# Performance work log

Hardware: AMD Instinct MI355X
Metric: run time of the kernel (lower is better)

The kernel has to match this reference:

```python
import jax, jax.numpy as jnp
import numpy as np
from jax.scipy.special import gammaln

EPS = 1e-8
N_SAMPLES = 2 ** 17
ATTACK_FULL_SIZE = 2048
CPD = 16
N_RES = 16
EXPR = 2
N_OSC = 2
N_GAUSS = 8
N_EVENTS = 4
FRAMES = 128
DEF_FRAMES = 128
N_LEVELS = 11  # log2(ATTACK_FULL_SIZE)


def unit_norm(x, axis=-1):
    return x / (jnp.linalg.norm(x, axis=axis, keepdims=True) + EPS)


def fft_convolve(a, b):
    # zero-pad to 2n to avoid circular wraparound, multiply spectra, crop to n
    n = a.shape[-1]
    fa = jnp.fft.rfft(a, n=2 * n, axis=-1)
    fb = jnp.fft.rfft(b, n=2 * n, axis=-1)
    return jnp.fft.irfft(fa * fb, n=2 * n, axis=-1)[..., :n]


def upsample_with_holes(x, size):
    # zero-insertion upsampling: place frames at stride `factor`
    factor = size // x.shape[-1]
    out = jnp.zeros(x.shape[:-1] + (size,), x.dtype)
    return out.at[..., ::factor].set(x)


def interpolate_last_axis(x, size):
    # linear interpolation, align_corners=False semantics (torch F.interpolate)
    n = x.shape[-1]
    scale = n / size
    src = jnp.clip((jnp.arange(size) + 0.5) * scale - 0.5, 0.0, n - 1.0)
    lo = jnp.floor(src).astype(jnp.int32)
    hi = jnp.minimum(lo + 1, n - 1)
    w = (src - lo).astype(x.dtype)
    return x[..., lo] * (1.0 - w) + x[..., hi] * w


def ensure_last_axis_length(x, size):
    n = x.shape[-1]
    if n == size:
        return x
    if n > size:
        return x[..., :size]
    return jnp.pad(x, [(0, 0)] * (x.ndim - 1) + [(0, size - n)])


def sparse_softmax(x):
    # hard one-hot forward, softmax straight-through backward
    sm = jax.nn.softmax(x, axis=-1)
    hard = jax.nn.one_hot(jnp.argmax(x, axis=-1), x.shape[-1], dtype=x.dtype)
    return hard + sm - jax.lax.stop_gradient(sm)


def hierarchical_dirac(p):
    # p: (..., L, 2) binary choices per level -> one-hot dirac of length 2**L
    sel = sparse_softmax(p)
    sig = sel[..., 0, :]
    for i in range(1, p.shape[-2]):
        sig = (sig[..., :, None] * sel[..., i, :][..., None, :]).reshape(*sig.shape[:-1], -1)
    return sig


def gamma_pdf(mean, std, n_elements):
    # gamma pdf on support (eps, 1], parameterized by mean/std
    t = jnp.linspace(EPS, 1.0, n_elements)
    k = (mean / (std + EPS)) ** 2
    rate = mean / (std ** 2 + EPS)
    k = k[..., None]
    rate = rate[..., None]
    logp = k * jnp.log(rate + EPS) + (k - 1.0) * jnp.log(t) - rate * t - gammaln(k)
    return jnp.exp(logp)


def damped_harmonic_oscillator(time, mass, damping, tension, x0):
    # underdamped closed-form solution, v0 = 0
    omega0_sq = tension / mass
    gamma = damping / (2.0 * mass)
    omega = jnp.sqrt(omega0_sq - gamma ** 2)
    A = x0
    B = gamma * x0 / omega
    return jnp.exp(-gamma * time) * (A * jnp.cos(omega * time) + B * jnp.sin(omega * time))


def dho_block(damping, mass, tension, disp, amps, tmod=None, scaling=None):
    time = jnp.linspace(0.0, 10.0, N_SAMPLES).reshape(1, 1, 1, N_SAMPLES)
    t = tension[..., None]  # (N_OSC, N_RES, EXPR, 1)
    if tmod is not None:
        t = t + tmod[0] * scaling  # broadcast -> (N_OSC, N_RES, EXPR, N_SAMPLES)
    x = damped_harmonic_oscillator(
        time,
        jax.nn.sigmoid(mass[..., None]) * 2.0,
        jax.nn.sigmoid(damping[..., None]) * 30.0,
        10.0 ** t,
        disp[..., None],
    )
    x = (x * amps).sum(axis=0)  # sum over oscillators
    return x.reshape(1, 1, N_RES, EXPR, N_SAMPLES)


def attack_envelopes(means, stds, amps, pos, overall_amp):
    m, s, a = jnp.abs(means), jnp.abs(stds), jnp.abs(amps)
    p = hierarchical_dirac(pos)  # (1,1,CPD,NG,2048)
    x = gamma_pdf(m, s, ATTACK_FULL_SIZE) * a[..., None]
    x = fft_convolve(x, p)
    x = x.sum(axis=2)  # (1,1,NG,2048)
    x = unit_norm(x)
    x = x * overall_amp[..., None]  # broadcast -> (1,1,CPD,NG,2048)
    x = x.sum(axis=-2)  # (1,1,CPD,2048)
    return x.reshape(CPD, ATTACK_FULL_SIZE)


def _forward(control_signal, deformations, ae_means, ae_stds, ae_amps, ae_pos,
             ae_overall_amp, dho_damping, dho_mass, dho_tension, dho_disp, dho_amp,
             influences, stack_mix, router, layer_mix, gains, attack_noise):
    b, ne, cpd, frames = control_signal.shape
    # --- DampedHarmonicOscillatorStack ---
    o1 = dho_block(dho_damping[0], dho_mass[0], dho_tension[0], dho_disp[0], dho_amp[0])
    o2 = dho_block(dho_damping[1], dho_mass[1], dho_tension[1], dho_disp[1], dho_amp[1], o1, influences[0])
    o3 = dho_block(dho_damping[2], dho_mass[2], dho_tension[2], dho_disp[2], dho_amp[2], o2, influences[1])
    res = (jnp.stack([o1, o2, o3], axis=-1) * jax.nn.softmax(stack_mix, axis=-1)).sum(axis=-1)
    res = unit_norm(res)
    # --- AttackEnvelopes ---
    ae = attack_envelopes(ae_means, ae_stds, ae_amps, ae_pos, ae_overall_amp)
    # --- execute_layer ---
    routed = jnp.einsum('becf,cr->berf', control_signal, router)
    before = routed
    res = unit_norm(res)  # execute_layer normalizes again
    routed = upsample_with_holes(routed.reshape(b, ne, N_RES, 1, frames), N_SAMPLES)
    # ae.shape[-1] == window_size, so materialize_attack_envelopes just multiplies noise
    impulse = ensure_last_axis_length(ae * attack_noise, N_SAMPLES).reshape(1, 1, cpd, 1, N_SAMPLES)
    routed = fft_convolve(impulse, routed)  # (1,ne,N_RES,1,S)
    cs = routed.reshape(1, ne, cpd, N_SAMPLES).sum(axis=1, keepdims=True)
    conv = fft_convolve(routed, res)  # (1,ne,N_RES,EXPR,S)
    base = jnp.zeros_like(deformations).at[:, :, 0:1, :].set(1.0)
    d = jax.nn.softmax(base + deformations, axis=-2)
    d = interpolate_last_axis(d.reshape(b, 1, 1, EXPR, -1), N_SAMPLES)
    x = (d * conv).sum(axis=-2)  # (1,ne,N_RES,S)
    mixes = jax.nn.softmax(layer_mix.reshape(1, 1, N_RES, 1, 1, 2), axis=-1)
    stacked = jnp.stack([routed, x.reshape(routed.shape)], axis=-1)
    x = (mixes * stacked).sum(axis=-1)
    x = x.reshape(1, 1, N_RES, -1)
    summed = jnp.tanh(x * jnp.abs(gains.reshape(1, 1, N_RES, 1)))
    summed = summed.sum(axis=-2, keepdims=True)
    return summed, before, cs


def setup_inputs() -> dict:
    key = jax.random.key(0)
    ks = jax.random.split(key, 20)
    u = lambda k, shape, lo, hi: jax.random.uniform(k, shape, jnp.float32, lo, hi)
    inp = {}
    inp['control_signal'] = jax.random.uniform(ks[0], (1, N_EVENTS, CPD, FRAMES), jnp.float32)
    inp['deformations'] = jax.random.normal(ks[1], (1, 1, EXPR, DEF_FRAMES), jnp.float32)
    inp['ae_means'] = u(ks[2], (1, 1, CPD, N_GAUSS), -6.0, 6.0)
    inp['ae_stds'] = u(ks[3], (1, 1, CPD, N_GAUSS), 0.5, 6.0)
    inp['ae_amps'] = u(ks[4], (1, 1, CPD, N_GAUSS), -6.0, 6.0)
    inp['ae_pos'] = u(ks[5], (1, 1, CPD, N_GAUSS, N_LEVELS, 2), -1.0, 1.0)
    inp['ae_overall_amp'] = u(ks[6], (1, 1, CPD, 1), -1.0, 1.0)
    inp['dho_damping'] = u(ks[7], (3, N_OSC, N_RES, EXPR), 0.5, 1.5)
    inp['dho_mass'] = u(ks[8], (3, N_OSC, N_RES, EXPR), -2.0, 2.0)
    inp['dho_tension'] = u(ks[9], (3, N_OSC, N_RES, EXPR), 4.0, 9.0)
    inp['dho_disp'] = u(ks[10], (3, N_OSC, N_RES, EXPR), -1.0, 2.0)
    inp['dho_amp'] = u(ks[11], (3, N_OSC, N_RES, EXPR, 1), -1.0, 1.0)
    inp['influences'] = u(ks[12], (2, N_OSC, N_RES, EXPR, 1), -0.01, 0.01)
    inp['stack_mix'] = u(ks[13], (1, 1, N_RES, EXPR, 1, 3), -1.0, 1.0)
    router = u(ks[14], (CPD, N_RES), -1.0, 1.0)
    mask = (jax.random.uniform(ks[15], (CPD, N_RES)) < 0.1).astype(jnp.float32)
    inp['router'] = router * mask
    inp['layer_mix'] = u(ks[16], (N_RES, 2), -1.0, 1.0)
    inp['gains'] = u(ks[17], (N_RES, 1), 0.01, 1.1)
    inp['attack_noise'] = u(ks[18], (CPD, ATTACK_FULL_SIZE), -1.0, 1.0)
    return inp


def reference(control_signal, deformations, ae_means, ae_stds, ae_amps, ae_pos,
              ae_overall_amp, dho_damping, dho_mass, dho_tension, dho_disp, dho_amp,
              influences, stack_mix, router, layer_mix, gains, attack_noise):
    return _forward(control_signal, deformations, ae_means, ae_stds, ae_amps, ae_pos,
                    ae_overall_amp, dho_damping, dho_mass, dho_tension, dho_disp, dho_amp,
                    influences, stack_mix, router, layer_mix, gains, attack_noise)
```

## Files before the change

### kernel.cpp

```cpp
#include <hip/hip_runtime.h>
#include <math.h>

#define NS 131072
#define EPSF 1e-8f

#define OFF_H      4194304u
#define OFF_IMP    8388608u
#define OFF_VG     8421376u
#define OFF_DW     8437760u
#define OFF_FV     8568832u
#define OFF_NORM   8577024u
#define OFF_GSS    8577056u
#define OFF_MIX0   8577064u
#define OFF_MIX1   8577080u
#define OFF_GABS   8577096u
#define OFF_W3     8577112u
#define OFF_PF     8577208u
#define OFF_PART   8578560u

#define AFRAG_USH  4194304u
#define ABF2_USH   4726784u

typedef __attribute__((ext_vector_type(8))) short short8;
typedef __attribute__((ext_vector_type(4))) float floatx4;
typedef __attribute__((ext_vector_type(4))) unsigned short ushort4v;

#define INV2PI 0.15915494309189535f

__device__ __forceinline__ float sigmf(float x) { return 1.0f / (1.0f + expf(-x)); }

__device__ __forceinline__ unsigned short f2bf(float x) {
  unsigned u = __float_as_uint(x);
  unsigned r = (u + 0x7FFFu + ((u >> 16) & 1u)) >> 16;
  return (unsigned short)r;
}

__global__ __launch_bounds__(256) void k0_prep(
    const float* __restrict__ csig, const float* __restrict__ deform,
    const float* __restrict__ ddmp, const float* __restrict__ dmas,
    const float* __restrict__ dten, const float* __restrict__ ddisp,
    const float* __restrict__ damp, const float* __restrict__ infl,
    const float* __restrict__ smix, const float* __restrict__ router,
    const float* __restrict__ lmix, const float* __restrict__ gains,
    float* __restrict__ wsf, float* __restrict__ out)
{
  int tid = threadIdx.x;
  int t = blockIdx.x * 256 + tid;
  {
    float4 z = {0.f, 0.f, 0.f, 0.f};
    *(float4*)&out[(size_t)t * 4] = z;
  }
  {
    float src = (t + 0.5f) * (1.0f / 1024.0f) - 0.5f;
    src = fminf(fmaxf(src, 0.0f), 127.0f);
    int lo = (int)src;
    int hi = min(lo + 1, 127);
    float w = src - (float)lo;
    float c0l = 1.0f / (1.0f + expf(deform[128 + lo] - (1.0f + deform[lo])));
    float c0h = 1.0f / (1.0f + expf(deform[128 + hi] - (1.0f + deform[hi])));
    wsf[OFF_DW + t] = c0l * (1.0f - w) + c0h * w;
  }
  if (blockIdx.x == 0) {
    for (int idx = tid; idx < 8192; idx += 256) {
      int e = idx >> 11, r = (idx >> 7) & 15, f = idx & 127;
      float s = 0.f;
      for (int c = 0; c < 16; ++c) s += csig[(e * 16 + c) * 128 + f] * router[c * 16 + r];
      wsf[OFF_FV + idx] = s;
      out[524288 + idx] = s;
    }
    if (tid < 8) wsf[OFF_GSS + tid] = 0.f;
    if (tid < 16) {
      int r = tid;
      float l0 = lmix[r * 2], l1 = lmix[r * 2 + 1];
      float m = fmaxf(l0, l1);
      float e0 = expf(l0 - m), e1 = expf(l1 - m), inv = 1.0f / (e0 + e1);
      wsf[OFF_MIX0 + r] = e0 * inv;
      wsf[OFF_MIX1 + r] = e1 * inv;
      wsf[OFF_GABS + r] = fabsf(gains[r]);
    }
    if (tid < 32) {
      int rx = tid, r = rx >> 1, x = rx & 1;
      float a0 = smix[rx * 3], a1 = smix[rx * 3 + 1], a2 = smix[rx * 3 + 2];
      float mm = fmaxf(a0, fmaxf(a1, a2));
      float e0 = expf(a0 - mm), e1 = expf(a1 - mm), e2 = expf(a2 - mm);
      float inv = 1.0f / (e0 + e1 + e2);
      wsf[OFF_W3 + rx * 3 + 0] = e0 * inv;
      wsf[OFF_W3 + rx * 3 + 1] = e1 * inv;
      wsf[OFF_W3 + rx * 3 + 2] = e2 * inv;
      float* pf = wsf + OFF_PF + rx * 32;
      for (int ent = 0; ent < 6; ++ent) {
        int b = ent >> 1, o = ent & 1;
        int id = ((b * 2 + o) * 16 + r) * 2 + x;
        float mass = 2.0f * sigmf(dmas[id]);
        float dampg = 30.0f * sigmf(ddmp[id]);
        float gam = dampg / (2.0f * mass);
        double W = exp((double)dten[id] * 2.302585092994046) / (double)mass;
        float x0v = ddisp[id];
        float ampv = damp[id];
        float infv = 0.f;
        if (b == 1) infv = infl[(o * 16 + r) * 2 + x];
        if (b == 2) infv = infl[((2 + o) * 16 + r) * 2 + x];
        pf[0 + ent]  = -gam;
        pf[6 + ent]  = ampv * x0v;
        pf[12 + ent] = gam * ampv * x0v;
        pf[18 + ent] = infv * 2.3025851f;
        if (b == 0) {
          double om = sqrt(W - (double)gam * (double)gam);
          pf[24 + o] = (float)((double)(gam * x0v * ampv) / om);
          pf[26 + o] = (float)(om * 0.15915494309189535);
        } else {
          pf[28 + ent - 2] = (float)W;
        }
      }
    }
  }
}

__global__ __launch_bounds__(256) void k1_dho(const float* __restrict__ wsf,
    unsigned short* __restrict__ resb, float* __restrict__ partials)
{
  int rx = blockIdx.y;
  int t = blockIdx.x * 256 + threadIdx.x;
  const float* pf = wsf + OFF_PF + rx * 32;
  float ttf = (float)t * (10.0f / 131071.0f);

  float o1v = 0.f;
#pragma unroll
  for (int o = 0; o < 2; ++o) {
    float fr = pf[26 + o] * ttf;
    fr -= rintf(fr);
    float sn = __builtin_amdgcn_sinf(fr);
    float cn = __builtin_amdgcn_cosf(fr);
    float ex = __expf(pf[o] * ttf);
    o1v += ex * (pf[6 + o] * cn + pf[24 + o] * sn);
  }
  float prev = o1v, o2v = 0.f, o3v = 0.f;
#pragma unroll
  for (int blk = 1; blk < 3; ++blk) {
    float acc = 0.f;
#pragma unroll
    for (int oo = 0; oo < 2; ++oo) {
      int o = blk * 2 + oo;
      float ng = pf[o];
      float p10 = __expf(prev * pf[18 + o]);
      float rad = __builtin_fmaf(pf[28 + o - 2], p10, -(ng * ng));
      float om = __builtin_amdgcn_sqrtf(rad);
      float fr = (om * INV2PI) * ttf;
      fr -= rintf(fr);
      float sn = __builtin_amdgcn_sinf(fr);
      float cn = __builtin_amdgcn_cosf(fr);
      float Bp = pf[12 + o] * __builtin_amdgcn_rcpf(om);
      float ex = __expf(ng * ttf);
      acc += ex * (pf[6 + o] * cn + Bp * sn);
    }
    if (blk == 1) o2v = acc; else o3v = acc;
    prev = acc;
  }
  const float* w3 = wsf + OFF_W3 + rx * 3;
  float rv = w3[0] * o1v + w3[1] * o2v + w3[2] * o3v;
  resb[(size_t)rx * NS + t] = f2bf(rv);

  __shared__ float bred[4];
  float sq = rv * rv;
#pragma unroll
  for (int off = 32; off; off >>= 1) sq += __shfl_down(sq, off, 64);
  if ((threadIdx.x & 63) == 0) bred[threadIdx.x >> 6] = sq;
  __syncthreads();
  if (threadIdx.x == 0)
    partials[rx * 512 + blockIdx.x] = bred[0] + bred[1] + bred[2] + bred[3];
}

__global__ __launch_bounds__(256) void k12_gauss_reduce(
    const float* __restrict__ means, const float* __restrict__ stds,
    const float* __restrict__ amps, const float* __restrict__ pos,
    const float* __restrict__ partials,
    float* __restrict__ vg, float* __restrict__ gss, float* __restrict__ norm_acc)
{
  int bid = blockIdx.x;
  int tid = threadIdx.x;
  __shared__ float kS[16], rateS[16], logAS[16], aS[16];
  __shared__ int dS[16];
  __shared__ float red[4];
  if (bid >= 64) {
    int rx = bid - 64;
    float s = partials[rx * 512 + tid] + partials[rx * 512 + 256 + tid];
#pragma unroll
    for (int off = 32; off; off >>= 1) s += __shfl_down(s, off, 64);
    if ((tid & 63) == 0) red[tid >> 6] = s;
    __syncthreads();
    if (tid == 0) norm_acc[rx] = red[0] + red[1] + red[2] + red[3];
    return;
  }
  int g = bid >> 3;
  int i = (bid & 7) * 256 + tid;
  if (tid < 16) {
    int c = tid, idx = c * 8 + g;
    double m = fabs((double)means[idx]);
    double s = fabs((double)stds[idx]);
    double k = m / (s + 1e-8); k = k * k;
    double rate = m / (s * s + 1e-8);
    double logA = k * log(rate + 1e-8) - lgamma(k);
    kS[c] = (float)k; rateS[c] = (float)rate; logAS[c] = (float)logA;
    aS[c] = fabsf(amps[idx]);
    int d = 0;
    for (int l = 0; l < 11; ++l) {
      float p0 = pos[(idx * 11 + l) * 2], p1 = pos[(idx * 11 + l) * 2 + 1];
      d = d * 2 + (p1 > p0 ? 1 : 0);
    }
    dS[c] = d;
  }
  __syncthreads();
  const float step = (float)((1.0 - 1e-8) / 2047.0);
  float v = 0.f;
  for (int c = 0; c < 16; ++c) {
    int mi = i - dS[c];
    if (mi >= 0) {
      float tm = 1e-8f + (float)mi * step;
      float lp = logAS[c] + (kS[c] - 1.0f) * __logf(tm) - rateS[c] * tm;
      v += aS[c] * __expf(lp);
    }
  }
  vg[g * 2048 + i] = v;
  float sumsq = v * v;
#pragma unroll
  for (int off = 32; off; off >>= 1) sumsq += __shfl_down(sumsq, off, 64);
  if ((tid & 63) == 0) red[tid >> 6] = sumsq;
  __syncthreads();
  if (tid == 0) atomicAdd(&gss[g], red[0] + red[1] + red[2] + red[3]);
}

__global__ __launch_bounds__(256) void k3_imp(
    const float* __restrict__ vg, const float* __restrict__ gss,
    const float* __restrict__ ovamp, const float* __restrict__ noise,
    float* __restrict__ imp)
{
  int c = blockIdx.y;
  int i = blockIdx.x * 256 + threadIdx.x;
  float S = 0.f;
#pragma unroll
  for (int g = 0; g < 8; ++g) S += vg[g * 2048 + i] / (sqrtf(gss[g]) + EPSF);
  imp[c * 2048 + i] = ovamp[c] * S * noise[c * 2048 + i];
}

__global__ __launch_bounds__(256) void kAA_frag(
    const float* __restrict__ imp, const float* __restrict__ wsf,
    unsigned short* __restrict__ abf, unsigned short* __restrict__ abf2)
{
  int bid = blockIdx.x;
  int tid = threadIdx.x;
  if (bid < 512) {
    int gid = bid * 256 + tid;
    int lane = gid & 63;
    int kt = (gid >> 6) & 3;
    int mt = (gid >> 8) & 7;
    int e  = (gid >> 11) & 3;
    int r  = (gid >> 13) & 15;
    int m = lane & 15, quad = lane >> 4;
    int base = mt * 16 + m - kt * 32 - quad * 8;
    const float* fve = wsf + OFF_FV + (e * 16 + r) * 128;
    short8 v;
#pragma unroll
    for (int j = 0; j < 8; ++j) {
      int f = base - j;
      unsigned short b = 0;
      if (f >= 0 && f < 128) b = f2bf(fve[f]);
      v[j] = (short)b;
    }
    *(short8*)&abf2[(size_t)gid * 8] = v;
  } else {
    int gid = (bid - 512) * 256 + tid;
    if (gid >= 66560) return;
    int r = gid / (65 * 64);
    int rem = gid % (65 * 64);
    int sc = rem >> 6, lane = rem & 63;
    int m = lane & 15, quad = lane >> 4;
    int qp = (quad < 2) ? quad : quad - 4;
    int base = 32 * sc + m - 8 * qp;
    short8 v;
#pragma unroll
    for (int j = 0; j < 8; ++j) {
      int idx = base - j;
      unsigned short b = 0;
      if (idx >= 0 && idx < 2048) b = f2bf(imp[r * 2048 + idx]);
      v[j] = (short)b;
    }
    *(short8*)&abf[(size_t)gid * 8] = v;
  }
}

__global__ __launch_bounds__(256) void k4_mfma(
    const unsigned short* __restrict__ resb, const unsigned short* __restrict__ abf,
    const float* __restrict__ norm_acc, const float* __restrict__ wsf,
    float* __restrict__ H)
{
  int rx = blockIdx.y, r = rx >> 1;
  int n0 = blockIdx.x * 256;
  __shared__ __align__(16) unsigned short Xs[9280];
  int tid = threadIdx.x;
  for (int i = tid; i < 1544; i += 256) {
    int q_rel = i >> 2, p4 = (i & 3) * 4;
    int q = n0 - 130 + q_rel;
    ushort4v v = {0, 0, 0, 0};
    if (q >= 0) v = *(const ushort4v*)&resb[(size_t)rx * NS + q * 16 + p4];
    *(ushort4v*)&Xs[q_rel * 24 + p4] = v;
  }
  __syncthreads();
  int lane = tid & 63, w = tid >> 6;
  int quad = lane >> 4, nl = lane & 15;
  float n1 = sqrtf(norm_acc[rx]);
  float s1 = 1.0f / (n1 + EPSF);
  float scale = s1 * (1.0f / (n1 * s1 + EPSF)) * wsf[OFF_MIX1 + r];
  const short8* af = (const short8*)(abf) + (size_t)r * 65 * 64 + lane;
  floatx4 acc0 = {0,0,0,0}, acc1 = {0,0,0,0}, acc2 = {0,0,0,0}, acc3 = {0,0,0,0};
  const char* xbase = (const char*)Xs + (size_t)(130 + w * 64 + nl - (quad >> 1)) * 48
                      + (quad & 1) * 16;
  short8 wbuf[25];
#pragma unroll
  for (int s = -24; s < 0; ++s)
    wbuf[s + 25] = *(const short8*)(xbase - 96 * s);
#pragma unroll
  for (int sc = 0; sc < 65; ++sc) {
    wbuf[sc % 25] = *(const short8*)(xbase - 96 * sc);
    short8 a = af[sc * 64];
    acc0 = __builtin_amdgcn_mfma_f32_16x16x32_bf16(a, wbuf[sc % 25],        acc0, 0, 0, 0);
    acc1 = __builtin_amdgcn_mfma_f32_16x16x32_bf16(a, wbuf[(sc + 17) % 25], acc1, 0, 0, 0);
    acc2 = __builtin_amdgcn_mfma_f32_16x16x32_bf16(a, wbuf[(sc + 9) % 25],  acc2, 0, 0, 0);
    acc3 = __builtin_amdgcn_mfma_f32_16x16x32_bf16(a, wbuf[(sc + 1) % 25],  acc3, 0, 0, 0);
  }
  float* hp = H + (size_t)rx * NS + 16 * (n0 + w * 64 + nl) + quad * 4;
#pragma unroll
  for (int i = 0; i < 4; ++i) {
    hp[i]       = acc0[i] * scale;
    hp[256 + i] = acc1[i] * scale;
    hp[512 + i] = acc2[i] * scale;
    hp[768 + i] = acc3[i] * scale;
  }
}

__global__ __launch_bounds__(256) void k6_mfma(
    const float* __restrict__ H, const float* __restrict__ imp,
    const unsigned short* __restrict__ abf2,
    const float* __restrict__ wsf, float* __restrict__ out)
{
  int r = blockIdx.y;
  int n0 = blockIdx.x * 32;
  int rm = r & 3, rq = r >> 2;
  int tid = threadIdx.x;
  int w = tid >> 6, lane = tid & 63;
  int wc = w & 1, wm = w >> 1;
  int quad = lane >> 4, n = lane & 15;
  int col = n0 + wc * 16 + n;

  __shared__ float fvs[4][128];
  for (int i = tid; i < 512; i += 256)
    fvs[i >> 7][i & 127] = wsf[OFF_FV + ((i >> 7) * 16 + r) * 128 + (i & 127)];
  __syncthreads();

  short8 bf0[4], bf1[4];
  const float* H0 = H + (size_t)(2 * r) * NS + col;
  const float* H1 = H + (size_t)(2 * r + 1) * NS + col;
#pragma unroll
  for (int kt = 0; kt < 4; ++kt) {
#pragma unroll
    for (int j = 0; j < 8; ++j) {
      int p = kt * 32 + quad * 8 + j;
      bf0[kt][j] = (short)f2bf(H0[(size_t)p * 1024]);
      bf1[kt][j] = (short)f2bf(H1[(size_t)p * 1024]);
    }
  }

  float d0r[4][4];
  const float* dwg = wsf + OFF_DW;
#pragma unroll
  for (int mi = 0; mi < 4; ++mi)
#pragma unroll
    for (int i = 0; i < 4; ++i) {
      int q = (wm * 4 + mi) * 16 + quad * 4 + i;
      d0r[mi][i] = dwg[q * 1024 + col];
    }

  float impA = imp[r * 2048 + col];
  float impB = imp[r * 2048 + 1024 + col];
  float mix0r = wsf[OFF_MIX0 + r];

  float tansum[4][4], csum[4][4];
#pragma unroll
  for (int mi = 0; mi < 4; ++mi)
#pragma unroll
    for (int i = 0; i < 4; ++i) { tansum[mi][i] = 0.f; csum[mi][i] = 0.f; }

  const short8* af = (const short8*)abf2;
  for (int e = 0; e < 4; ++e) {
    float ge = wsf[OFF_GABS + 4 * e + rq];
    const short8* afe = af + ((size_t)(r * 4 + e) * 32) * 64 + lane;
#pragma unroll
    for (int mi = 0; mi < 4; ++mi) {
      int mt = wm * 4 + mi;
      floatx4 acc0 = {0, 0, 0, 0}, acc1 = {0, 0, 0, 0};
#pragma unroll
      for (int kt = 0; kt < 4; ++kt) {
        short8 a = afe[(mt * 4 + kt) * 64];
        acc0 = __builtin_amdgcn_mfma_f32_16x16x32_bf16(a, bf0[kt], acc0, 0, 0, 0);
        acc1 = __builtin_amdgcn_mfma_f32_16x16x32_bf16(a, bf1[kt], acc1, 0, 0, 0);
      }
#pragma unroll
      for (int i = 0; i < 4; ++i) {
        int q = mt * 16 + quad * 4 + i;
        float fq = fvs[e][q];
        float fqm = (q > 0) ? fvs[e][q - 1] : 0.f;
        float rsv = fq * impA + fqm * impB;
        csum[mi][i] += rsv;
        float d0 = d0r[mi][i];
        float conv = d0 * acc0[i] + (1.0f - d0) * acc1[i];
        float z = (mix0r * rsv + conv) * ge;
        float e2 = __expf(2.0f * z);
        tansum[mi][i] += 1.0f - 2.0f / (e2 + 1.0f);
      }
    }
  }
#pragma unroll
  for (int mi = 0; mi < 4; ++mi)
#pragma unroll
    for (int i = 0; i < 4; ++i) {
      int q = (wm * 4 + mi) * 16 + quad * 4 + i;
      atomicAdd(&out[(size_t)rm * NS + q * 1024 + col], tansum[mi][i]);
      out[532480 + (size_t)r * NS + q * 1024 + col] = csum[mi][i];
    }
}

extern "C" void kernel_launch(void* const* d_in, const int* in_sizes, int n_in,
                              void* d_out, int out_size, void* d_ws, size_t ws_size,
                              hipStream_t stream) {
  const float* csig   = (const float*)d_in[0];
  const float* deform = (const float*)d_in[1];
  const float* aem    = (const float*)d_in[2];
  const float* aes    = (const float*)d_in[3];
  const float* aea    = (const float*)d_in[4];
  const float* aep    = (const float*)d_in[5];
  const float* aeo    = (const float*)d_in[6];
  const float* ddmp   = (const float*)d_in[7];
  const float* dmas   = (const float*)d_in[8];
  const float* dten   = (const float*)d_in[9];
  const float* ddisp  = (const float*)d_in[10];
  const float* damp   = (const float*)d_in[11];
  const float* infl   = (const float*)d_in[12];
  const float* smix   = (const float*)d_in[13];
  const float* router = (const float*)d_in[14];
  const float* lmix   = (const float*)d_in[15];
  const float* gains  = (const float*)d_in[16];
  const float* anoise = (const float*)d_in[17];

  float*  wsf = (float*)d_ws;
  unsigned short* resb = (unsigned short*)d_ws;
  unsigned short* abf  = (unsigned short*)d_ws + AFRAG_USH;
  unsigned short* abf2 = (unsigned short*)d_ws + ABF2_USH;
  float*  out = (float*)d_out;

  k0_prep<<<512, 256, 0, stream>>>(csig, deform, ddmp, dmas, dten, ddisp, damp,
                                   infl, smix, router, lmix, gains, wsf, out);
  k1_dho<<<dim3(512, 32), 256, 0, stream>>>(wsf, resb, wsf + OFF_PART);
  k12_gauss_reduce<<<96, 256, 0, stream>>>(aem, aes, aea, aep, wsf + OFF_PART,
                                           wsf + OFF_VG, wsf + OFF_GSS,
                                           wsf + OFF_NORM);
  k3_imp<<<dim3(8, 16), 256, 0, stream>>>(wsf + OFF_VG, wsf + OFF_GSS, aeo, anoise,
                                          wsf + OFF_IMP);
  kAA_frag<<<772, 256, 0, stream>>>(wsf + OFF_IMP, wsf, abf, abf2);
  k4_mfma<<<dim3(32, 32), 256, 0, stream>>>(resb, abf, wsf + OFF_NORM, wsf,
                                            wsf + OFF_H);
  k6_mfma<<<dim3(32, 16), 256, 0, stream>>>(wsf + OFF_H, wsf + OFF_IMP, abf2, wsf, out);
}
```

Baseline: 195.8 us.

## Fuse small prep kernels and store intermediate H as bf16

Merges the prep, gamma-envelope, impulse and fragment-packing kernels, cutting the launch sequence from seven kernels to five. The gaussian sum-of-squares now goes through per-block partials instead of atomics. The intermediate H buffer is written as bf16 rather than fp32, which halves its write and read traffic between the two MFMA stages and moves the conversion into the producer. The fused impulse fragment path recomputes the gaussian mixture per element, adding some redundant arithmetic.

After: 176.8 us. -9.7%, faster.

```diff
diff --git a/kernel.cpp b/kernel.cpp
--- a/kernel.cpp
+++ b/kernel.cpp
@@ -4,22 +4,22 @@
 #define NS 131072
 #define EPSF 1e-8f
 
-#define OFF_H      4194304u
 #define OFF_IMP    8388608u
 #define OFF_VG     8421376u
 #define OFF_DW     8437760u
 #define OFF_FV     8568832u
 #define OFF_NORM   8577024u
-#define OFF_GSS    8577056u
 #define OFF_MIX0   8577064u
 #define OFF_MIX1   8577080u
 #define OFF_GABS   8577096u
 #define OFF_W3     8577112u
 #define OFF_PF     8577208u
 #define OFF_PART   8578560u
+#define OFF_GSSP   8594944u
 
 #define AFRAG_USH  4194304u
 #define ABF2_USH   4726784u
+#define HB_USH     8388608u
 
 typedef __attribute__((ext_vector_type(8))) short short8;
 typedef __attribute__((ext_vector_type(4))) float floatx4;
@@ -35,84 +35,152 @@
   return (unsigned short)r;
 }
 
-__global__ __launch_bounds__(256) void k0_prep(
+__global__ __launch_bounds__(256) void kA_prep(
     const float* __restrict__ csig, const float* __restrict__ deform,
     const float* __restrict__ ddmp, const float* __restrict__ dmas,
     const float* __restrict__ dten, const float* __restrict__ ddisp,
     const float* __restrict__ damp, const float* __restrict__ infl,
     const float* __restrict__ smix, const float* __restrict__ router,
     const float* __restrict__ lmix, const float* __restrict__ gains,
-    float* __restrict__ wsf, float* __restrict__ out)
+    const float* __restrict__ means, const float* __restrict__ stds,
+    const float* __restrict__ amps, const float* __restrict__ pos,
+    float* __restrict__ wsf, unsigned short* __restrict__ abf2,
+    float* __restrict__ out)
 {
   int tid = threadIdx.x;
-  int t = blockIdx.x * 256 + tid;
-  {
-    float4 z = {0.f, 0.f, 0.f, 0.f};
-    *(float4*)&out[(size_t)t * 4] = z;
-  }
-  {
-    float src = (t + 0.5f) * (1.0f / 1024.0f) - 0.5f;
-    src = fminf(fmaxf(src, 0.0f), 127.0f);
-    int lo = (int)src;
-    int hi = min(lo + 1, 127);
-    float w = src - (float)lo;
-    float c0l = 1.0f / (1.0f + expf(deform[128 + lo] - (1.0f + deform[lo])));
-    float c0h = 1.0f / (1.0f + expf(deform[128 + hi] - (1.0f + deform[hi])));
-    wsf[OFF_DW + t] = c0l * (1.0f - w) + c0h * w;
-  }
-  if (blockIdx.x == 0) {
-    for (int idx = tid; idx < 8192; idx += 256) {
-      int e = idx >> 11, r = (idx >> 7) & 15, f = idx & 127;
+  int bid = blockIdx.x;
+  if (bid < 512) {
+    int t = bid * 256 + tid;
+    {
+      float4 z = {0.f, 0.f, 0.f, 0.f};
+      *(float4*)&out[(size_t)t * 4] = z;
+    }
+    {
+      float src = (t + 0.5f) * (1.0f / 1024.0f) - 0.5f;
+      src = fminf(fmaxf(src, 0.0f), 127.0f);
+      int lo = (int)src;
+      int hi = min(lo + 1, 127);
+      float w = src - (float)lo;
+      float c0l = 1.0f / (1.0f + expf(deform[128 + lo] - (1.0f + deform[lo])));
+      float c0h = 1.0f / (1.0f + expf(deform[128 + hi] - (1.0f + deform[hi])));
+      wsf[OFF_DW + t] = c0l * (1.0f - w) + c0h * w;
+    }
+    int mt = bid & 7, e = (bid >> 3) & 3, r = (bid >> 5) & 15;
+    __shared__ float fvrow[128];
+    if (tid < 128) {
       float s = 0.f;
-      for (int c = 0; c < 16; ++c) s += csig[(e * 16 + c) * 128 + f] * router[c * 16 + r];
-      wsf[OFF_FV + idx] = s;
-      out[524288 + idx] = s;
-    }
-    if (tid < 8) wsf[OFF_GSS + tid] = 0.f;
+      for (int c = 0; c < 16; ++c)
+        s += csig[(e * 16 + c) * 128 + tid] * router[c * 16 + r];
+      fvrow[tid] = s;
+      if (mt == 0) {
+        wsf[OFF_FV + (e * 16 + r) * 128 + tid] = s;
+        out[524288 + (e * 16 + r) * 128 + tid] = s;
+      }
+    }
+    __syncthreads();
+    {
+      int gid = bid * 256 + tid;
+      int lane = gid & 63;
+      int kt = (gid >> 6) & 3;
+      int m = lane & 15, quad = lane >> 4;
+      int base = mt * 16 + m - kt * 32 - quad * 8;
+      short8 v;
+#pragma unroll
+      for (int j = 0; j < 8; ++j) {
+        int f = base - j;
+        unsigned short b = 0;
+        if (f >= 0 && f < 128) b = f2bf(fvrow[f]);
+        v[j] = (short)b;
+      }
+      *(short8*)&abf2[(size_t)gid * 8] = v;
+    }
+    if (bid == 0) {
+      if (tid < 16) {
+        int r2 = tid;
+        float l0 = lmix[r2 * 2], l1 = lmix[r2 * 2 + 1];
+        float mx = fmaxf(l0, l1);
+        float e0 = expf(l0 - mx), e1 = expf(l1 - mx), inv = 1.0f / (e0 + e1);
+        wsf[OFF_MIX0 + r2] = e0 * inv;
+        wsf[OFF_MIX1 + r2] = e1 * inv;
+        wsf[OFF_GABS + r2] = fabsf(gains[r2]);
+      }
+      if (tid < 32) {
+        int rx = tid, r2 = rx >> 1, x = rx & 1;
+        float a0 = smix[rx * 3], a1 = smix[rx * 3 + 1], a2 = smix[rx * 3 + 2];
+        float mm = fmaxf(a0, fmaxf(a1, a2));
+        float e0 = expf(a0 - mm), e1 = expf(a1 - mm), e2 = expf(a2 - mm);
+        float inv = 1.0f / (e0 + e1 + e2);
+        wsf[OFF_W3 + rx * 3 + 0] = e0 * inv;
+        wsf[OFF_W3 + rx * 3 + 1] = e1 * inv;
+        wsf[OFF_W3 + rx * 3 + 2] = e2 * inv;
+        float* pf = wsf + OFF_PF + rx * 32;
+        for (int ent = 0; ent < 6; ++ent) {
+          int b = ent >> 1, o = ent & 1;
+          int id = ((b * 2 + o) * 16 + r2) * 2 + x;
+          float mass = 2.0f * sigmf(dmas[id]);
+          float dampg = 30.0f * sigmf(ddmp[id]);
+          float gam = dampg / (2.0f * mass);
+          double W = exp((double)dten[id] * 2.302585092994046) / (double)mass;
+          float x0v = ddisp[id];
+          float ampv = damp[id];
+          float infv = 0.f;
+          if (b == 1) infv = infl[(o * 16 + r2) * 2 + x];
+          if (b == 2) infv = infl[((2 + o) * 16 + r2) * 2 + x];
+          pf[0 + ent]  = -gam;
+          pf[6 + ent]  = ampv * x0v;
+          pf[12 + ent] = gam * ampv * x0v;
+          pf[18 + ent] = infv * 2.3025851f;
+          if (b == 0) {
+            double om = sqrt(W - (double)gam * (double)gam);
+            pf[24 + o] = (float)((double)(gam * x0v * ampv) / om);
+            pf[26 + o] = (float)(om * 0.15915494309189535);
+          } else {
+            pf[28 + ent - 2] = (float)W;
+          }
+        }
+      }
+    }
+  } else {
+    int gb = bid - 512;
+    int g = gb >> 3;
+    int i = (gb & 7) * 256 + tid;
+    __shared__ float kS[16], rateS[16], logAS[16], aS[16];
+    __shared__ int dS[16];
+    __shared__ float red[4];
     if (tid < 16) {
-      int r = tid;
-      float l0 = lmix[r * 2], l1 = lmix[r * 2 + 1];
-      float m = fmaxf(l0, l1);
-      float e0 = expf(l0 - m), e1 = expf(l1 - m), inv = 1.0f / (e0 + e1);
-      wsf[OFF_MIX0 + r] = e0 * inv;
-      wsf[OFF_MIX1 + r] = e1 * inv;
-      wsf[OFF_GABS + r] = fabsf(gains[r]);
-    }
-    if (tid < 32) {
-      int rx = tid, r = rx >> 1, x = rx & 1;
-      float a0 = smix[rx * 3], a1 = smix[rx * 3 + 1], a2 = smix[rx * 3 + 2];
-      float mm = fmaxf(a0, fmaxf(a1, a2));
-      float e0 = expf(a0 - mm), e1 = expf(a1 - mm), e2 = expf(a2 - mm);
-      float inv = 1.0f / (e0 + e1 + e2);
-      wsf[OFF_W3 + rx * 3 + 0] = e0 * inv;
-      wsf[OFF_W3 + rx * 3 + 1] = e1 * inv;
-      wsf[OFF_W3 + rx * 3 + 2] = e2 * inv;
-      float* pf = wsf + OFF_PF + rx * 32;
-      for (int ent = 0; ent < 6; ++ent) {
-        int b = ent >> 1, o = ent & 1;
-        int id = ((b * 2 + o) * 16 + r) * 2 + x;
-        float mass = 2.0f * sigmf(dmas[id]);
-        float dampg = 30.0f * sigmf(ddmp[id]);
-        float gam = dampg / (2.0f * mass);
-        double W = exp((double)dten[id] * 2.302585092994046) / (double)mass;
-        float x0v = ddisp[id];
-        float ampv = damp[id];
-        float infv = 0.f;
-        if (b == 1) infv = infl[(o * 16 + r) * 2 + x];
-        if (b == 2) infv = infl[((2 + o) * 16 + r) * 2 + x];
-        pf[0 + ent]  = -gam;
-        pf[6 + ent]  = ampv * x0v;
-        pf[12 + ent] = gam * ampv * x0v;
-        pf[18 + ent] = infv * 2.3025851f;
-        if (b == 0) {
-          double om = sqrt(W - (double)gam * (double)gam);
-          pf[24 + o] = (float)((double)(gam * x0v * ampv) / om);
-          pf[26 + o] = (float)(om * 0.15915494309189535);
-        } else {
-          pf[28 + ent - 2] = (float)W;
-        }
-      }
-    }
+      int c = tid, idx = c * 8 + g;
+      double m = fabs((double)means[idx]);
+      double s = fabs((double)stds[idx]);
+      double k = m / (s + 1e-8); k = k * k;
+      double rate = m / (s * s + 1e-8);
+      double logA = k * log(rate + 1e-8) - lgamma(k);
+      kS[c] = (float)k; rateS[c] = (float)rate; logAS[c] = (float)logA;
+      aS[c] = fabsf(amps[idx]);
+      int d = 0;
+      for (int l = 0; l < 11; ++l) {
+        float p0 = pos[(idx * 11 + l) * 2], p1 = pos[(idx * 11 + l) * 2 + 1];
+        d = d * 2 + (p1 > p0 ? 1 : 0);
+      }
+      dS[c] = d;
+    }
+    __syncthreads();
+    const float step = (float)((1.0 - 1e-8) / 2047.0);
+    float v = 0.f;
+    for (int c = 0; c < 16; ++c) {
+      int mi = i - dS[c];
+      if (mi >= 0) {
+        float tm = 1e-8f + (float)mi * step;
+        float lp = logAS[c] + (kS[c] - 1.0f) * __logf(tm) - rateS[c] * tm;
+        v += aS[c] * __expf(lp);
+      }
+    }
+    wsf[OFF_VG + g * 2048 + i] = v;
+    float sumsq = v * v;
+#pragma unroll
+    for (int off = 32; off; off >>= 1) sumsq += __shfl_down(sumsq, off, 64);
+    if ((tid & 63) == 0) red[tid >> 6] = sumsq;
+    __syncthreads();
+    if (tid == 0) wsf[OFF_GSSP + gb] = red[0] + red[1] + red[2] + red[3];
   }
 }
 
@@ -170,144 +238,87 @@
     partials[rx * 512 + blockIdx.x] = bred[0] + bred[1] + bred[2] + bred[3];
 }
 
-__global__ __launch_bounds__(256) void k12_gauss_reduce(
-    const float* __restrict__ means, const float* __restrict__ stds,
-    const float* __restrict__ amps, const float* __restrict__ pos,
-    const float* __restrict__ partials,
-    float* __restrict__ vg, float* __restrict__ gss, float* __restrict__ norm_acc)
+__global__ __launch_bounds__(256) void kB_mid(
+    const float* __restrict__ ovamp, const float* __restrict__ noise,
+    float* __restrict__ wsf, unsigned short* __restrict__ abf)
 {
   int bid = blockIdx.x;
   int tid = threadIdx.x;
-  __shared__ float kS[16], rateS[16], logAS[16], aS[16];
-  __shared__ int dS[16];
-  __shared__ float red[4];
-  if (bid >= 64) {
-    int rx = bid - 64;
+  if (bid < 32) {
+    int rx = bid;
+    const float* partials = wsf + OFF_PART;
+    __shared__ float red[4];
     float s = partials[rx * 512 + tid] + partials[rx * 512 + 256 + tid];
 #pragma unroll
     for (int off = 32; off; off >>= 1) s += __shfl_down(s, off, 64);
     if ((tid & 63) == 0) red[tid >> 6] = s;
     __syncthreads();
-    if (tid == 0) norm_acc[rx] = red[0] + red[1] + red[2] + red[3];
+    if (tid == 0) wsf[OFF_NORM + rx] = red[0] + red[1] + red[2] + red[3];
     return;
   }
-  int g = bid >> 3;
-  int i = (bid & 7) * 256 + tid;
-  if (tid < 16) {
-    int c = tid, idx = c * 8 + g;
-    double m = fabs((double)means[idx]);
-    double s = fabs((double)stds[idx]);
-    double k = m / (s + 1e-8); k = k * k;
-    double rate = m / (s * s + 1e-8);
-    double logA = k * log(rate + 1e-8) - lgamma(k);
-    kS[c] = (float)k; rateS[c] = (float)rate; logAS[c] = (float)logA;
-    aS[c] = fabsf(amps[idx]);
-    int d = 0;
-    for (int l = 0; l < 11; ++l) {
-      float p0 = pos[(idx * 11 + l) * 2], p1 = pos[(idx * 11 + l) * 2 + 1];
-      d = d * 2 + (p1 > p0 ? 1 : 0);
-    }
-    dS[c] = d;
+  __shared__ float wS[8];
+  if (tid < 8) {
+    float g8 = 0.f;
+#pragma unroll
+    for (int u = 0; u < 8; ++u) g8 += wsf[OFF_GSSP + tid * 8 + u];
+    wS[tid] = 1.0f / (sqrtf(g8) + EPSF);
   }
   __syncthreads();
-  const float step = (float)((1.0 - 1e-8) / 2047.0);
-  float v = 0.f;
-  for (int c = 0; c < 16; ++c) {
-    int mi = i - dS[c];
-    if (mi >= 0) {
-      float tm = 1e-8f + (float)mi * step;
-      float lp = logAS[c] + (kS[c] - 1.0f) * __logf(tm) - rateS[c] * tm;
-      v += aS[c] * __expf(lp);
-    }
-  }
-  vg[g * 2048 + i] = v;
-  float sumsq = v * v;
-#pragma unroll
-  for (int off = 32; off; off >>= 1) sumsq += __shfl_down(sumsq, off, 64);
-  if ((tid & 63) == 0) red[tid >> 6] = sumsq;
-  __syncthreads();
-  if (tid == 0) atomicAdd(&gss[g], red[0] + red[1] + red[2] + red[3]);
-}
-
-__global__ __launch_bounds__(256) void k3_imp(
-    const float* __restrict__ vg, const float* __restrict__ gss,
-    const float* __restrict__ ovamp, const float* __restrict__ noise,
-    float* __restrict__ imp)
-{
-  int c = blockIdx.y;
-  int i = blockIdx.x * 256 + threadIdx.x;
-  float S = 0.f;
-#pragma unroll
-  for (int g = 0; g < 8; ++g) S += vg[g * 2048 + i] / (sqrtf(gss[g]) + EPSF);
-  imp[c * 2048 + i] = ovamp[c] * S * noise[c * 2048 + i];
-}
-
-__global__ __launch_bounds__(256) void kAA_frag(
-    const float* __restrict__ imp, const float* __restrict__ wsf,
-    unsigned short* __restrict__ abf, unsigned short* __restrict__ abf2)
-{
-  int bid = blockIdx.x;
-  int tid = threadIdx.x;
-  if (bid < 512) {
-    int gid = bid * 256 + tid;
-    int lane = gid & 63;
-    int kt = (gid >> 6) & 3;
-    int mt = (gid >> 8) & 7;
-    int e  = (gid >> 11) & 3;
-    int r  = (gid >> 13) & 15;
-    int m = lane & 15, quad = lane >> 4;
-    int base = mt * 16 + m - kt * 32 - quad * 8;
-    const float* fve = wsf + OFF_FV + (e * 16 + r) * 128;
-    short8 v;
-#pragma unroll
-    for (int j = 0; j < 8; ++j) {
-      int f = base - j;
-      unsigned short b = 0;
-      if (f >= 0 && f < 128) b = f2bf(fve[f]);
-      v[j] = (short)b;
-    }
-    *(short8*)&abf2[(size_t)gid * 8] = v;
-  } else {
-    int gid = (bid - 512) * 256 + tid;
-    if (gid >= 66560) return;
-    int r = gid / (65 * 64);
-    int rem = gid % (65 * 64);
-    int sc = rem >> 6, lane = rem & 63;
-    int m = lane & 15, quad = lane >> 4;
-    int qp = (quad < 2) ? quad : quad - 4;
-    int base = 32 * sc + m - 8 * qp;
-    short8 v;
-#pragma unroll
-    for (int j = 0; j < 8; ++j) {
-      int idx = base - j;
-      unsigned short b = 0;
-      if (idx >= 0 && idx < 2048) b = f2bf(imp[r * 2048 + idx]);
-      v[j] = (short)b;
-    }
-    *(short8*)&abf[(size_t)gid * 8] = v;
-  }
+  const float* vg = wsf + OFF_VG;
+  if (bid < 160) {
+    int idx0 = bid - 32;
+    int c = idx0 >> 3;
+    int i = (idx0 & 7) * 256 + tid;
+    float S = 0.f;
+#pragma unroll
+    for (int g = 0; g < 8; ++g) S += vg[g * 2048 + i] * wS[g];
+    wsf[OFF_IMP + c * 2048 + i] = ovamp[c] * S * noise[c * 2048 + i];
+    return;
+  }
+  int gid = (bid - 160) * 256 + tid;
+  if (gid >= 66560) return;
+  int r = gid / (65 * 64);
+  int rem = gid % (65 * 64);
+  int sc = rem >> 6, lane = rem & 63;
+  int m = lane & 15, quad = lane >> 4;
+  int qp = (quad < 2) ? quad : quad - 4;
+  int base = 32 * sc + m - 8 * qp;
+  float oa = ovamp[r];
+  short8 v;
+#pragma unroll
+  for (int j = 0; j < 8; ++j) {
+    int idx = base - j;
+    unsigned short b = 0;
+    if (idx >= 0 && idx < 2048) {
+      float S = 0.f;
+#pragma unroll
+      for (int g = 0; g < 8; ++g) S += vg[g * 2048 + idx] * wS[g];
+      b = f2bf(oa * S * noise[r * 2048 + idx]);
+    }
+    v[j] = (short)b;
+  }
+  *(short8*)&abf[(size_t)gid * 8] = v;
 }
 
 __global__ __launch_bounds__(256) void k4_mfma(
     const unsigned short* __restrict__ resb, const unsigned short* __restrict__ abf,
-    const float* __restrict__ norm_acc, const float* __restrict__ wsf,
-    float* __restrict__ H)
+    const float* __restrict__ wsf, unsigned short* __restrict__ Hb)
 {
   int rx = blockIdx.y, r = rx >> 1;
   int n0 = blockIdx.x * 256;
   __shared__ __align__(16) unsigned short Xs[9280];
   int tid = threadIdx.x;
-  for (int i = tid; i < 1544; i += 256) {
-    int q_rel = i >> 2, p4 = (i & 3) * 4;
+  for (int i = tid; i < 772; i += 256) {
+    int q_rel = i >> 1, p8 = (i & 1) * 8;
     int q = n0 - 130 + q_rel;
-    ushort4v v = {0, 0, 0, 0};
-    if (q >= 0) v = *(const ushort4v*)&resb[(size_t)rx * NS + q * 16 + p4];
-    *(ushort4v*)&Xs[q_rel * 24 + p4] = v;
+    short8 v = {0, 0, 0, 0, 0, 0, 0, 0};
+    if (q >= 0) v = *(const short8*)&resb[(size_t)rx * NS + q * 16 + p8];
+    *(short8*)&Xs[q_rel * 24 + p8] = v;
   }
   __syncthreads();
   int lane = tid & 63, w = tid >> 6;
   int quad = lane >> 4, nl = lane & 15;
-  float n1 = sqrtf(norm_acc[rx]);
+  float n1 = sqrtf(wsf[OFF_NORM + rx]);
   float s1 = 1.0f / (n1 + EPSF);
   float scale = s1 * (1.0f / (n1 * s1 + EPSF)) * wsf[OFF_MIX1 + r];
   const short8* af = (const short8*)(abf) + (size_t)r * 65 * 64 + lane;
@@ -327,18 +338,23 @@
     acc2 = __builtin_amdgcn_mfma_f32_16x16x32_bf16(a, wbuf[(sc + 9) % 25],  acc2, 0, 0, 0);
     acc3 = __builtin_amdgcn_mfma_f32_16x16x32_bf16(a, wbuf[(sc + 1) % 25],  acc3, 0, 0, 0);
   }
-  float* hp = H + (size_t)rx * NS + 16 * (n0 + w * 64 + nl) + quad * 4;
+  unsigned short* hp = Hb + (size_t)rx * NS + 16 * (n0 + w * 64 + nl) + quad * 4;
+  ushort4v h0, h1, h2, h3;
 #pragma unroll
   for (int i = 0; i < 4; ++i) {
-    hp[i]       = acc0[i] * scale;
-    hp[256 + i] = acc1[i] * scale;
-    hp[512 + i] = acc2[i] * scale;
-    hp[768 + i] = acc3[i] * scale;
-  }
+    h0[i] = f2bf(acc0[i] * scale);
+    h1[i] = f2bf(acc1[i] * scale);
+    h2[i] = f2bf(acc2[i] * scale);
+    h3[i] = f2bf(acc3[i] * scale);
+  }
+  *(ushort4v*)(hp)       = h0;
+  *(ushort4v*)(hp + 256) = h1;
+  *(ushort4v*)(hp + 512) = h2;
+  *(ushort4v*)(hp + 768) = h3;
 }
 
 __global__ __launch_bounds__(256) void k6_mfma(
-    const float* __restrict__ H, const float* __restrict__ imp,
+    const unsigned short* __restrict__ Hb, const float* __restrict__ imp,
     const unsigned short* __restrict__ abf2,
     const float* __restrict__ wsf, float* __restrict__ out)
 {
@@ -357,15 +373,15 @@
   __syncthreads();
 
   short8 bf0[4], bf1[4];
-  const float* H0 = H + (size_t)(2 * r) * NS + col;
-  const float* H1 = H + (size_t)(2 * r + 1) * NS + col;
+  const unsigned short* H0 = Hb + (size_t)(2 * r) * NS + col;
+  const unsigned short* H1 = Hb + (size_t)(2 * r + 1) * NS + col;
 #pragma unroll
   for (int kt = 0; kt < 4; ++kt) {
 #pragma unroll
     for (int j = 0; j < 8; ++j) {
       int p = kt * 32 + quad * 8 + j;
-      bf0[kt][j] = (short)f2bf(H0[(size_t)p * 1024]);
-      bf1[kt][j] = (short)f2bf(H1[(size_t)p * 1024]);
+      bf0[kt][j] = (short)H0[(size_t)p * 1024];
+      bf1[kt][j] = (short)H1[(size_t)p * 1024];
     }
   }
 
@@ -454,18 +470,14 @@
   unsigned short* resb = (unsigned short*)d_ws;
   unsigned short* abf  = (unsigned short*)d_ws + AFRAG_USH;
   unsigned short* abf2 = (unsigned short*)d_ws + ABF2_USH;
+  unsigned short* Hb   = (unsigned short*)d_ws + HB_USH;
   float*  out = (float*)d_out;
 
-  k0_prep<<<512, 256, 0, stream>>>(csig, deform, ddmp, dmas, dten, ddisp, damp,
-                                   infl, smix, router, lmix, gains, wsf, out);
+  kA_prep<<<576, 256, 0, stream>>>(csig, deform, ddmp, dmas, dten, ddisp, damp,
+                                   infl, smix, router, lmix, gains,
+                                   aem, aes, aea, aep, wsf, abf2, out);
   k1_dho<<<dim3(512, 32), 256, 0, stream>>>(wsf, resb, wsf + OFF_PART);
-  k12_gauss_reduce<<<96, 256, 0, stream>>>(aem, aes, aea, aep, wsf + OFF_PART,
-                                           wsf + OFF_VG, wsf + OFF_GSS,
-                                           wsf + OFF_NORM);
-  k3_imp<<<dim3(8, 16), 256, 0, stream>>>(wsf + OFF_VG, wsf + OFF_GSS, aeo, anoise,
-                                          wsf + OFF_IMP);
-  kAA_frag<<<772, 256, 0, stream>>>(wsf + OFF_IMP, wsf, abf, abf2);
-  k4_mfma<<<dim3(32, 32), 256, 0, stream>>>(resb, abf, wsf + OFF_NORM, wsf,
-                                            wsf + OFF_H);
-  k6_mfma<<<dim3(32, 16), 256, 0, stream>>>(wsf + OFF_H, wsf + OFF_IMP, abf2, wsf, out);
-}
+  kB_mid<<<420, 256, 0, stream>>>(aeo, anoise, wsf, abf);
+  k4_mfma<<<dim3(32, 32), 256, 0, stream>>>(resb, abf, wsf, Hb);
+  k6_mfma<<<dim3(32, 16), 256, 0, stream>>>(Hb, wsf + OFF_IMP, abf2, wsf, out);
+}
```
